# Kernel tuning notes

Hardware: AMD Instinct MI355X
Metric: run time of the kernel (lower is better)

The kernel has to match this reference:

```python
import jax, jax.numpy as jnp
import numpy as np

N_NODES = 20000
D_FEAT = 256
N_SUPPORT = 3
N_EDGES = 320000
OUT_DIM = 256


def setup_inputs() -> dict:
    key = jax.random.key(0)
    k1, k2, k3, k4, k5 = jax.random.split(key, 5)
    x = jax.random.normal(k1, (N_NODES, D_FEAT), dtype=jnp.float32)
    edge_src = jax.random.randint(k2, (N_SUPPORT, N_EDGES), 0, N_NODES, dtype=jnp.int64 if jax.config.jax_enable_x64 else jnp.int32).astype(jnp.int32)
    edge_dst = jax.random.randint(k3, (N_SUPPORT, N_EDGES), 0, N_NODES, dtype=jnp.int32)
    edge_w = jax.random.uniform(k4, (N_SUPPORT, N_EDGES), dtype=jnp.float32)
    # dense weight over concatenated supports: (support * input_dim, output_dim)
    W = jax.random.normal(k5, (N_SUPPORT * D_FEAT, OUT_DIM), dtype=jnp.float32) * (1.0 / np.sqrt(N_SUPPORT * D_FEAT))
    return {"x": x, "edge_src": edge_src, "edge_dst": edge_dst, "edge_w": edge_w, "W": W}


def reference(x, edge_src, edge_dst, edge_w, W):
    # supports_i = A_i @ x  (sparse adjacency as weighted edge list, per support)
    n = x.shape[0]
    supports = []
    for s in range(edge_src.shape[0]):  # small fixed number of relations
        msgs = x[edge_src[s]] * edge_w[s][:, None]              # [E, d]
        supports.append(jax.ops.segment_sum(msgs, edge_dst[s], num_segments=n))
    h = jnp.concatenate(supports, axis=1)                        # [N, support*d]
    # activation='linear' -> identity; bias=False
    return h @ W                                                 # [N, output_dim]
```

## Files before the change

kernel.cpp:

```cpp
#include <hip/hip_runtime.h>

#define N_NODES 20000
#define D_FEAT 256
#define N_SUPPORT 3
#define N_EDGES 320000
#define OUT_DIM 256
#define TOTAL_E (N_SUPPORT * N_EDGES)
#define CAPX 16
#define NWIN 8
#define KDIM (N_SUPPORT * D_FEAT)
#define NBUCKET (N_SUPPORT * N_NODES)
#define GM_ROWS 128
#define GM_BLOCKS ((N_NODES + GM_ROWS - 1) / GM_ROWS)

typedef __attribute__((ext_vector_type(8))) short short8;
typedef __attribute__((ext_vector_type(8))) unsigned short ushort8;
typedef __attribute__((ext_vector_type(4))) float f32x4;

__device__ inline unsigned short f2bf(float f) {
    unsigned int u = __float_as_uint(f);
    u += 0x7fff + ((u >> 16) & 1);
    return (unsigned short)(u >> 16);
}

#define NB_X (N_NODES / 16)
#define NB_W (N_SUPPORT * D_FEAT)
#define NB_F (TOTAL_E / 256)

__global__ void __launch_bounds__(256) prep1(const float* __restrict__ x, const float* __restrict__ W,
        unsigned int* __restrict__ xq, float* __restrict__ scl, unsigned short* __restrict__ wt) {
    const int bid = blockIdx.x;
    const int tid = threadIdx.x;
    if (bid < NB_X) {
        const int wid = tid >> 6;
        const int lane = tid & 63;
        const int row0 = bid * 16 + wid * 4;
        float4 v[4];
        float m[4];
#pragma unroll
        for (int r = 0; r < 4; ++r) {
            v[r] = ((const float4*)x)[(size_t)(row0 + r) * 64 + lane];
            m[r] = fmaxf(fmaxf(fabsf(v[r].x), fabsf(v[r].y)), fmaxf(fabsf(v[r].z), fabsf(v[r].w)));
        }
#pragma unroll
        for (int d = 1; d < 64; d <<= 1) {
#pragma unroll
            for (int r = 0; r < 4; ++r) m[r] = fmaxf(m[r], __shfl_xor(m[r], d, 64));
        }
#pragma unroll
        for (int r = 0; r < 4; ++r) {
            const float inv = (m[r] > 0.f) ? 127.0f / m[r] : 0.f;
            int q0 = (int)rintf(v[r].x * inv) + 128;
            int q1 = (int)rintf(v[r].y * inv) + 128;
            int q2 = (int)rintf(v[r].z * inv) + 128;
            int q3 = (int)rintf(v[r].w * inv) + 128;
            unsigned int pk = (unsigned int)q0 | ((unsigned int)q1 << 8)
                            | ((unsigned int)q2 << 16) | ((unsigned int)q3 << 24);
            xq[(size_t)(row0 + r) * 64 + lane] = pk;
            if (lane == 0) scl[row0 + r] = m[r] * (1.0f / 127.0f);
        }
    } else {
        const int row = bid - NB_X;
        const int s = row >> 8, k = row & 255;
        wt[((size_t)s * OUT_DIM + tid) * D_FEAT + k] = f2bf(W[(size_t)row * OUT_DIM + tid]);
    }
}

__global__ void __launch_bounds__(256) fill_win(const int* __restrict__ src,
        const int* __restrict__ dst, const float* __restrict__ w, const float* __restrict__ scl,
        int* __restrict__ cur8, unsigned int* __restrict__ ep1) {
    const int i = blockIdx.x * 256 + threadIdx.x;
    if (i >= TOTAL_E) return;
    const int win = blockIdx.x & (NWIN - 1);
    const int s = i / N_EDGES;
    const int sv = src[i];
    const int b = s * N_NODES + dst[i];
    const int pos = atomicAdd(&cur8[b * NWIN + win], 1);
    if (pos < CAPX) {
        const float wq = w[i] * scl[sv];
        ep1[(size_t)b * (NWIN * CAPX) + win * CAPX + pos] =
            (unsigned int)sv | (((unsigned int)f2bf(wq)) << 16);
    }
}

#define PROC(p) {                                                              \
    const unsigned int sv_ = (p) & 0xFFFFu;                                    \
    const uint2 u_ = *(const uint2*)(xq + ((size_t)sv_ << 8) + xoff);          \
    const float wv_ = __uint_as_float((p) & 0xFFFF0000u);                      \
    sw += wv_;                                                                 \
    _Pragma("unroll")                                                          \
    for (int j = 0; j < 4; ++j) {                                              \
        const int sh = 8 * j;                                                  \
        a[j]     += wv_ * (float)((u_.x >> sh) & 0xffu);                       \
        a[4 + j] += wv_ * (float)((u_.y >> sh) & 0xffu);                       \
    }                                                                          \
}

__global__ void __launch_bounds__(256) aggregate(
        const unsigned char* __restrict__ xq, const int* __restrict__ cur8,
        const unsigned int* __restrict__ ep1, unsigned short* __restrict__ hb) {
    const int b = blockIdx.x * 8 + (threadIdx.x >> 5);
    const int l32 = threadIdx.x & 31;
    const int xoff = l32 * 8;
    const int s = b / N_NODES;
    const int node = b - s * N_NODES;

    int myc = 0;
    if (l32 < NWIN) {
        int c = cur8[b * NWIN + l32];
        myc = (c > CAPX) ? CAPX : c;
    }
    int c[NWIN];
#pragma unroll
    for (int w = 0; w < NWIN; ++w) c[w] = __shfl(myc, w, 32);

    const unsigned int* eb = ep1 + (size_t)b * (NWIN * CAPX);

    uint4 g[NWIN];
#pragma unroll
    for (int w = 0; w < NWIN; ++w) g[w] = *(const uint4*)(eb + w * CAPX);

    float a[8];
#pragma unroll
    for (int j = 0; j < 8; ++j) a[j] = 0.f;
    float sw = 0.f;

#pragma unroll
    for (int w = 0; w < NWIN; ++w) {
        const int cw = c[w];
        const unsigned int p0 = (cw > 0) ? g[w].x : 0u;
        const unsigned int p1 = (cw > 1) ? g[w].y : 0u;
        const unsigned int p2 = (cw > 2) ? g[w].z : 0u;
        const unsigned int p3 = (cw > 3) ? g[w].w : 0u;
        PROC(p0); PROC(p1); PROC(p2); PROC(p3);
        if (cw > 4) {
            for (int it = 4; it < cw; ++it) {
                const unsigned int pe = eb[w * CAPX + it];
                PROC(pe);
            }
        }
    }

    ushort8 o;
    const float bias = 128.f * sw;
#pragma unroll
    for (int j = 0; j < 8; ++j) o[j] = f2bf(a[j] - bias);
    *(ushort8*)(hb + (size_t)node * KDIM + s * D_FEAT + xoff) = o;
}

__global__ void __launch_bounds__(512) gemm_h(
        const unsigned short* __restrict__ hb, const unsigned short* __restrict__ wt,
        float* __restrict__ out) {
    __shared__ unsigned short bs[OUT_DIM][136];
    const int n0 = blockIdx.x * GM_ROWS;
    const int wid = threadIdx.x >> 6;
    const int lane = threadIdx.x & 63;
    const int cit = lane & 15;
    const int kgrp = (lane >> 4) * 8;
    const bool valid = (n0 + wid * 16) < N_NODES;
    const int arow_idx = valid ? (n0 + wid * 16 + cit) : 0;
    const short* arow = (const short*)hb + (size_t)arow_idx * KDIM + kgrp;

    f32x4 acc[16];
#pragma unroll
    for (int j = 0; j < 16; ++j) acc[j] = (f32x4){0.f, 0.f, 0.f, 0.f};

    for (int kc = 0; kc < 6; ++kc) {
        const int s = kc >> 1;
        const int kb = (kc & 1) * 128;
        if (kc) __syncthreads();
        for (int i = threadIdx.x; i < 4096; i += 512) {
            const int n = i >> 4;
            const int k8 = (i & 15) << 3;
            *(ushort8*)&bs[n][k8] =
                *(const ushort8*)(wt + ((size_t)s * OUT_DIM + n) * D_FEAT + kb + k8);
        }
        __syncthreads();

#pragma unroll
        for (int ks = 0; ks < 4; ++ks) {
            short8 av = *(const short8*)(arow + kc * 128 + ks * 32);
#pragma unroll
            for (int nt = 0; nt < 16; ++nt) {
                short8 bv = *(const short8*)&bs[nt * 16 + cit][ks * 32 + kgrp];
                acc[nt] = __builtin_amdgcn_mfma_f32_16x16x32_bf16(av, bv, acc[nt], 0, 0, 0);
            }
        }
    }

    if (valid) {
        const int rbase = (lane >> 4) * 4;
#pragma unroll
        for (int nt = 0; nt < 16; ++nt) {
            const int col = nt * 16 + cit;
#pragma unroll
            for (int r = 0; r < 4; ++r) {
                out[(size_t)(n0 + wid * 16 + rbase + r) * OUT_DIM + col] = acc[nt][r];
            }
        }
    }
}

extern "C" void kernel_launch(void* const* d_in, const int* in_sizes, int n_in,
                              void* d_out, int out_size, void* d_ws, size_t ws_size,
                              hipStream_t stream) {
    const float* x        = (const float*)d_in[0];
    const int*   edge_src = (const int*)d_in[1];
    const int*   edge_dst = (const int*)d_in[2];
    const float* edge_w   = (const float*)d_in[3];
    const float* W        = (const float*)d_in[4];
    float* out = (float*)d_out;

    char* ws = (char*)d_ws;
    unsigned int*   xq    = (unsigned int*)(ws);
    float*          scl   = (float*)(ws + 5120000);
    unsigned short* wt    = (unsigned short*)(ws + 5200000);
    int*            cur8  = (int*)(ws + 5593216);
    unsigned int*   ep1   = (unsigned int*)(ws + 7513216);
    unsigned short* hb    = (unsigned short*)(ws + 38233216);

    hipMemsetAsync(cur8, 0, 1920000, stream);

    prep1<<<NB_X + NB_W, 256, 0, stream>>>(x, W, xq, scl, wt);
    fill_win<<<NB_F, 256, 0, stream>>>(edge_src, edge_dst, edge_w, scl, cur8, ep1);

    aggregate<<<NBUCKET / 8, 256, 0, stream>>>((const unsigned char*)xq, cur8, ep1, hb);

    gemm_h<<<GM_BLOCKS, 512, 0, stream>>>(hb, wt, out);
}
```

Baseline: 144.6 us.

## Embed per-window counters in 64-byte edge lines laid out window-major

Each (window, bucket) edge list becomes a 16-word line whose first word is the atomic counter, followed by up to 15 packed edges. The layout changes from bucket-major to window-major. The aggregate kernel no longer reads a separate counter array and shuffles counts; it reads the counter together with the first three edges in one 16-byte load, then pulls further 16-byte chunks only when needed. The cost is a much larger memset (the whole 30 MB edge buffer instead of a 1.9 MB counter array), and per-window capacity drops from 16 to 15.

```diff
diff --git a/kernel.cpp b/kernel.cpp
--- a/kernel.cpp
+++ b/kernel.cpp
@@ -6,8 +6,9 @@
 #define N_EDGES 320000
 #define OUT_DIM 256
 #define TOTAL_E (N_SUPPORT * N_EDGES)
-#define CAPX 16
 #define NWIN 8
+#define LWORDS 16
+#define CAPX 15
 #define KDIM (N_SUPPORT * D_FEAT)
 #define NBUCKET (N_SUPPORT * N_NODES)
 #define GM_ROWS 128
@@ -68,18 +69,18 @@
 
 __global__ void __launch_bounds__(256) fill_win(const int* __restrict__ src,
         const int* __restrict__ dst, const float* __restrict__ w, const float* __restrict__ scl,
-        int* __restrict__ cur8, unsigned int* __restrict__ ep1) {
+        unsigned int* __restrict__ ep1) {
     const int i = blockIdx.x * 256 + threadIdx.x;
     if (i >= TOTAL_E) return;
     const int win = blockIdx.x & (NWIN - 1);
     const int s = i / N_EDGES;
     const int sv = src[i];
     const int b = s * N_NODES + dst[i];
-    const int pos = atomicAdd(&cur8[b * NWIN + win], 1);
+    unsigned int* line = ep1 + ((size_t)win * NBUCKET + b) * LWORDS;
+    const unsigned int pos = atomicAdd(line, 1u);
     if (pos < CAPX) {
         const float wq = w[i] * scl[sv];
-        ep1[(size_t)b * (NWIN * CAPX) + win * CAPX + pos] =
-            (unsigned int)sv | (((unsigned int)f2bf(wq)) << 16);
+        line[1 + pos] = (unsigned int)sv | (((unsigned int)f2bf(wq)) << 16);
     }
 }
 
@@ -97,28 +98,18 @@
 }
 
 __global__ void __launch_bounds__(256) aggregate(
-        const unsigned char* __restrict__ xq, const int* __restrict__ cur8,
-        const unsigned int* __restrict__ ep1, unsigned short* __restrict__ hb) {
+        const unsigned char* __restrict__ xq, const unsigned int* __restrict__ ep1,
+        unsigned short* __restrict__ hb) {
     const int b = blockIdx.x * 8 + (threadIdx.x >> 5);
     const int l32 = threadIdx.x & 31;
     const int xoff = l32 * 8;
     const int s = b / N_NODES;
     const int node = b - s * N_NODES;
 
-    int myc = 0;
-    if (l32 < NWIN) {
-        int c = cur8[b * NWIN + l32];
-        myc = (c > CAPX) ? CAPX : c;
-    }
-    int c[NWIN];
-#pragma unroll
-    for (int w = 0; w < NWIN; ++w) c[w] = __shfl(myc, w, 32);
-
-    const unsigned int* eb = ep1 + (size_t)b * (NWIN * CAPX);
-
-    uint4 g[NWIN];
-#pragma unroll
-    for (int w = 0; w < NWIN; ++w) g[w] = *(const uint4*)(eb + w * CAPX);
+    uint4 h0[NWIN];
+#pragma unroll
+    for (int w = 0; w < NWIN; ++w)
+        h0[w] = *(const uint4*)(ep1 + ((size_t)w * NBUCKET + b) * LWORDS);
 
     float a[8];
 #pragma unroll
@@ -127,16 +118,30 @@
 
 #pragma unroll
     for (int w = 0; w < NWIN; ++w) {
-        const int cw = c[w];
-        const unsigned int p0 = (cw > 0) ? g[w].x : 0u;
-        const unsigned int p1 = (cw > 1) ? g[w].y : 0u;
-        const unsigned int p2 = (cw > 2) ? g[w].z : 0u;
-        const unsigned int p3 = (cw > 3) ? g[w].w : 0u;
-        PROC(p0); PROC(p1); PROC(p2); PROC(p3);
-        if (cw > 4) {
-            for (int it = 4; it < cw; ++it) {
-                const unsigned int pe = eb[w * CAPX + it];
-                PROC(pe);
+        unsigned int cnt = h0[w].x; if (cnt > CAPX) cnt = CAPX;
+        if (cnt > 0) PROC(h0[w].y);
+        if (cnt > 1) PROC(h0[w].z);
+        if (cnt > 2) PROC(h0[w].w);
+        if (cnt > 3) {
+            const unsigned int* lp = ep1 + ((size_t)w * NBUCKET + b) * LWORDS + 4;
+            uint4 t = *(const uint4*)lp;
+            PROC(t.x);
+            if (cnt > 4) PROC(t.y);
+            if (cnt > 5) PROC(t.z);
+            if (cnt > 6) PROC(t.w);
+            if (cnt > 7) {
+                uint4 t2 = *(const uint4*)(lp + 4);
+                PROC(t2.x);
+                if (cnt > 8) PROC(t2.y);
+                if (cnt > 9) PROC(t2.z);
+                if (cnt > 10) PROC(t2.w);
+                if (cnt > 11) {
+                    uint4 t3 = *(const uint4*)(lp + 8);
+                    PROC(t3.x);
+                    if (cnt > 12) PROC(t3.y);
+                    if (cnt > 13) PROC(t3.z);
+                    if (cnt > 14) PROC(t3.w);
+                }
             }
         }
     }
@@ -215,16 +220,15 @@
     unsigned int*   xq    = (unsigned int*)(ws);
     float*          scl   = (float*)(ws + 5120000);
     unsigned short* wt    = (unsigned short*)(ws + 5200000);
-    int*            cur8  = (int*)(ws + 5593216);
-    unsigned int*   ep1   = (unsigned int*)(ws + 7513216);
-    unsigned short* hb    = (unsigned short*)(ws + 38233216);
-
-    hipMemsetAsync(cur8, 0, 1920000, stream);
+    unsigned int*   ep1   = (unsigned int*)(ws + 5593216);
+    unsigned short* hb    = (unsigned short*)(ws + 36313216);
+
+    hipMemsetAsync(ep1, 0, 30720000, stream);
 
     prep1<<<NB_X + NB_W, 256, 0, stream>>>(x, W, xq, scl, wt);
-    fill_win<<<NB_F, 256, 0, stream>>>(edge_src, edge_dst, edge_w, scl, cur8, ep1);
-
-    aggregate<<<NBUCKET / 8, 256, 0, stream>>>((const unsigned char*)xq, cur8, ep1, hb);
+    fill_win<<<NB_F, 256, 0, stream>>>(edge_src, edge_dst, edge_w, scl, ep1);
+
+    aggregate<<<NBUCKET / 8, 256, 0, stream>>>((const unsigned char*)xq, ep1, hb);
 
     gemm_h<<<GM_BLOCKS, 512, 0, stream>>>(hb, wt, out);
 }
```

After: 149.9 us. 3.7% more time.

## Store edge windows window-major and unroll overflow slots with vector loads

Applied to the files above, without the earlier changes.

Moves the per-bucket counters and edge-slot arrays from bucket-major to window-major order, so consecutive buckets within one window sit next to each other for both the atomic fill and the aggregate reads. In aggregate, every lane now reads the eight counters directly instead of using shuffles. Slots beyond the first four are read with uint4 vector loads in a fully unrolled chain, and empty slots are skipped by branches rather than processed as zero entries. This is meant to cut strided and scalar memory traffic and wasted gathers, at the cost of more divergent branches and redundant counter loads per lane.

```diff
diff --git a/kernel.cpp b/kernel.cpp
--- a/kernel.cpp
+++ b/kernel.cpp
@@ -75,10 +75,10 @@
     const int s = i / N_EDGES;
     const int sv = src[i];
     const int b = s * N_NODES + dst[i];
-    const int pos = atomicAdd(&cur8[b * NWIN + win], 1);
+    const int pos = atomicAdd(&cur8[win * NBUCKET + b], 1);
     if (pos < CAPX) {
         const float wq = w[i] * scl[sv];
-        ep1[(size_t)b * (NWIN * CAPX) + win * CAPX + pos] =
+        ep1[((size_t)win * NBUCKET + b) * CAPX + pos] =
             (unsigned int)sv | (((unsigned int)f2bf(wq)) << 16);
     }
 }
@@ -105,20 +105,17 @@
     const int s = b / N_NODES;
     const int node = b - s * N_NODES;
 
-    int myc = 0;
-    if (l32 < NWIN) {
-        int c = cur8[b * NWIN + l32];
-        myc = (c > CAPX) ? CAPX : c;
-    }
     int c[NWIN];
 #pragma unroll
-    for (int w = 0; w < NWIN; ++w) c[w] = __shfl(myc, w, 32);
-
-    const unsigned int* eb = ep1 + (size_t)b * (NWIN * CAPX);
+    for (int w = 0; w < NWIN; ++w) {
+        int cc = cur8[w * NBUCKET + b];
+        c[w] = (cc > CAPX) ? CAPX : cc;
+    }
 
     uint4 g[NWIN];
 #pragma unroll
-    for (int w = 0; w < NWIN; ++w) g[w] = *(const uint4*)(eb + w * CAPX);
+    for (int w = 0; w < NWIN; ++w)
+        g[w] = *(const uint4*)(ep1 + ((size_t)w * NBUCKET + b) * CAPX);
 
     float a[8];
 #pragma unroll
@@ -128,15 +125,30 @@
 #pragma unroll
     for (int w = 0; w < NWIN; ++w) {
         const int cw = c[w];
-        const unsigned int p0 = (cw > 0) ? g[w].x : 0u;
-        const unsigned int p1 = (cw > 1) ? g[w].y : 0u;
-        const unsigned int p2 = (cw > 2) ? g[w].z : 0u;
-        const unsigned int p3 = (cw > 3) ? g[w].w : 0u;
-        PROC(p0); PROC(p1); PROC(p2); PROC(p3);
+        if (cw > 0) PROC(g[w].x);
+        if (cw > 1) PROC(g[w].y);
+        if (cw > 2) PROC(g[w].z);
+        if (cw > 3) PROC(g[w].w);
         if (cw > 4) {
-            for (int it = 4; it < cw; ++it) {
-                const unsigned int pe = eb[w * CAPX + it];
-                PROC(pe);
+            const unsigned int* lp = ep1 + ((size_t)w * NBUCKET + b) * CAPX + 4;
+            uint4 t = *(const uint4*)lp;
+            PROC(t.x);
+            if (cw > 5) PROC(t.y);
+            if (cw > 6) PROC(t.z);
+            if (cw > 7) PROC(t.w);
+            if (cw > 8) {
+                uint4 t2 = *(const uint4*)(lp + 4);
+                PROC(t2.x);
+                if (cw > 9) PROC(t2.y);
+                if (cw > 10) PROC(t2.z);
+                if (cw > 11) PROC(t2.w);
+                if (cw > 12) {
+                    uint4 t3 = *(const uint4*)(lp + 8);
+                    PROC(t3.x);
+                    if (cw > 13) PROC(t3.y);
+                    if (cw > 14) PROC(t3.z);
+                    if (cw > 15) PROC(t3.w);
+                }
             }
         }
     }
```

Result: no change. 145.4 us (+0.5%).
